# Kernel optimization log

Measured on AMD Instinct MI355X. Metric: run time of the kernel, lower is better.

Reference implementation:

```python
import jax, jax.numpy as jnp
import numpy as np

NC = 5        # num_class
NS = 2        # n_sigma
MAX_ID = 3    # candidate instance ids per class: 1..MAX_ID
W_INST, W_VAR, W_SEED = 1.0, 10.0, 1.0
GRID = 1024   # size of the registered xym buffer
H = W = 768
CLASS_WEIGHT = np.ones((NC,), np.float32)


def _xym(h, w):
    # buffer built at GRID resolution, then sliced [0:h, 0:w] (matches torch)
    base = jnp.linspace(0.0, 1.0, GRID)
    xm = jnp.broadcast_to(base[None, :w], (h, w))  # x varies along width
    ym = jnp.broadcast_to(base[:h, None], (h, w))  # y varies along height
    return jnp.stack([xm, ym], 0)  # [2,h,w]


def _lovasz_flat(logits, labels_f):
    # standard flat Lovasz hinge
    signs = 2.0 * labels_f - 1.0
    errors = 1.0 - logits * signs
    perm = jnp.argsort(-errors)  # descending errors
    errors_sorted = errors[perm]
    gt_sorted = labels_f[perm]
    gts = jnp.sum(gt_sorted)
    inter = gts - jnp.cumsum(gt_sorted)
    union = gts + jnp.cumsum(1.0 - gt_sorted)
    jac = 1.0 - inter / union
    jac = jnp.concatenate([jac[:1], jac[1:] - jac[:-1]])
    return jnp.dot(jax.nn.relu(errors_sorted), jax.lax.stop_gradient(jac))


def _per_image(pred, inst, lab, xyf, cw):
    h, w = lab.shape
    n = h * w
    embf = jnp.tanh(pred[0:2]).reshape(2, n) + xyf          # spatial embedding [2,N]
    sigf = pred[2:2 + NS].reshape(NS, n)                     # sigma [NS,N]
    seedf = jax.nn.sigmoid(pred[2 + NS:2 + NS + NC]).reshape(NC, n)  # seed maps [NC,N]
    labf = lab.reshape(n)
    instf = inst.reshape(n)

    cls = jnp.arange(1, NC + 1)
    # background seed loss per class: sum(seed^2) over pixels where label != cl
    bg = labf[None, :] != cls[:, None]
    seed_bg = jnp.sum(jnp.where(bg, seedf, 0.0) ** 2)

    cl_pair = jnp.repeat(cls, MAX_ID)                       # [P]
    id_pair = jnp.tile(jnp.arange(1, MAX_ID + 1), NC)       # [P]

    def per_inst(cl, iid):
        ci = cl - 1
        m = (labf == cl) & (instf == iid)                   # [N]
        mf = m.astype(embf.dtype)
        cnt = jnp.sum(mf)
        valid = cnt > 0
        cnts = jnp.maximum(cnt, 1.0)
        # approximate medoid: per-dim lower median of masked coords,
        # then masked pixel closest to the median
        xy_sorted = jnp.sort(jnp.where(m[None, :], xyf, 2.0), axis=1)
        mid = jnp.maximum((cnt.astype(jnp.int32) - 1) // 2, 0)
        med = jnp.take(xy_sorted, mid, axis=1)              # [2]
        d = jnp.sum((xyf - med[:, None]) ** 2, axis=0)
        imin = jnp.argmin(jnp.where(m, d, jnp.inf))
        center = jnp.take(xyf, imin, axis=1)                # [2], constant wrt params
        s_mean = jnp.sum(sigf * mf[None, :], axis=1) / cnts  # [NS]
        var = jnp.sum(mf[None, :] * (sigf - jax.lax.stop_gradient(s_mean)[:, None]) ** 2) / (cnts * NS)
        s = jnp.exp(s_mean * 10.0)                           # [NS]
        dist = jnp.exp(-jnp.sum((embf - center[:, None]) ** 2 * s[:, None], axis=0))  # [N]
        lov = _lovasz_flat(dist * 2.0 - 1.0, mf)
        seedc = jnp.take(seedf, ci, axis=0)
        seed_in = jnp.sum(mf * (seedc - jax.lax.stop_gradient(dist)) ** 2)
        return valid, var, lov, seed_in

    valid, var, lov, seed_in = jax.vmap(per_inst)(cl_pair, id_pair)
    vf = valid.astype(embf.dtype)
    objs = jnp.maximum(jnp.sum(vf), 1.0)
    w_pair = jnp.take(cw, cl_pair - 1)
    seed_loss = (seed_bg + jnp.sum(w_pair * seed_in * vf)) / n
    return (W_INST * jnp.sum(lov * vf) / objs
            + W_VAR * jnp.sum(var * vf) / objs
            + W_SEED * seed_loss)


def setup_inputs() -> dict:
    key = jax.random.key(0)
    k1, k2, k3 = jax.random.split(key, 3)
    prediction = jax.random.normal(k1, (2, 2 + NS + NC, H, W), dtype=jnp.float32)
    instances = jax.random.randint(k2, (2, H, W), 0, MAX_ID + 1, dtype=jnp.int32)
    labels = jax.random.randint(k3, (2, H, W), 0, NC + 1, dtype=jnp.int32)
    return {"prediction": prediction, "instances": instances, "labels": labels}


def reference(prediction, instances, labels):
    xyf = _xym(H, W).reshape(2, H * W)
    cw = jnp.asarray(CLASS_WEIGHT)
    losses = jax.vmap(lambda p, i, l: _per_image(p, i, l, xyf, cw))(prediction, instances, labels)
    return jnp.mean(losses)
```

## Files before the change

kernel.cpp:

```cpp
#include <hip/hip_runtime.h>
#include <cstddef>
#include <cstdint>


#define HH 768
#define WW 768
#define NPIX (HH*WW)
#define NCL 5
#define MAXID 3
#define PAIRS (NCL*MAXID)
#define NIMG 2
#define NCH 9
#define BINS 256
#define NSH 8
#define HPXB 1152
#define HNB (NPIX/HPXB)
#define XW 256
#define YH 16
#define TX 3
#define TY 48
#define BPI (TX*TY)
#define ANB 64
#define APXB (NPIX/ANB)

struct WS {
  alignas(8) unsigned int hall8[NSH][NIMG][PAIRS][2][BINS];
  float seedpart[NIMG][PAIRS][64];
  unsigned int lovdone;
  unsigned int zpad0;
  unsigned long long argkey[NIMG][PAIRS];
  float varsum[NIMG][PAIRS];
  float seedin[NIMG][PAIRS];
  float medx[NIMG][PAIRS], medy[NIMG][PAIRS];
  float s0a[NIMG][PAIRS], s1a[NIMG][PAIRS];
  float sm0a[NIMG][PAIRS], sm1a[NIMG][PAIRS];
  float validf[NIMG][PAIRS], cntf[NIMG][PAIRS];
  float lov[NIMG][PAIRS];
  float seedT[NIMG], seedOwn[NIMG];
  unsigned int cnt[NIMG][PAIRS];
  alignas(16) float4 emb4[NIMG][NPIX];
  unsigned char pridx[NIMG][NPIX];
  alignas(64) unsigned short colpart[NIMG][PAIRS][WW][TY];
  alignas(64) unsigned short rowpart[NIMG][PAIRS][HH][TX];
  float sig0part[NIMG][PAIRS][BPI];
  float sig1part[NIMG][PAIRS][BPI];
  float sq0part[NIMG][PAIRS][BPI];
  float sq1part[NIMG][PAIRS][BPI];
  float sTpart[NIMG][BPI];
  float sOpart[NIMG][BPI];
};

__device__ __forceinline__ float basef(int i) {
  return (float)i * (1.0f / 1023.0f);
}
__device__ __forceinline__ int pair_of(int l, int it) {
  return (l >= 1 && l <= NCL && it >= 1 && it <= MAXID) ? (l - 1) * MAXID + (it - 1) : -1;
}
__device__ __forceinline__ float fast_sigmoid(float z) {
  return __fdividef(1.f, 1.f + __expf(-z));
}
__device__ __forceinline__ float fast_tanh(float x) {
  float xc = fminf(fmaxf(x, -15.f), 15.f);
  float e = __expf(2.f * xc);
  return __fdividef(e - 1.f, e + 1.f);
}
__device__ __forceinline__ float vget(float4 v, int k) {
  return (k == 0) ? v.x : (k == 1) ? v.y : (k == 2) ? v.z : v.w;
}
__device__ __forceinline__ int iget(int4 v, int k) {
  return (k == 0) ? v.x : (k == 1) ? v.y : (k == 2) ? v.z : v.w;
}

__global__ __launch_bounds__(512) void k_pass1(const float* __restrict__ pred,
                                               const int* __restrict__ inst,
                                               const int* __restrict__ lab,
                                               WS* __restrict__ ws) {
  int img = blockIdx.z;
  int xt = blockIdx.x, yt = blockIdx.y;
  int x0 = xt * XW;
  int y0 = yt * YH;
  int tid = threadIdx.x, lane = tid & 63, wv = tid >> 6;

  {
    const int ZN = (int)(offsetof(WS, argkey) / 4);
    int bid = (blockIdx.z * TY + blockIdx.y) * TX + blockIdx.x;
    int idx = bid * 512 + tid;
    if (idx < ZN) ((unsigned int*)ws)[idx] = 0u;
    if (bid == 0 && tid < NIMG * PAIRS)
      ((unsigned long long*)ws->argkey)[tid] = ~0ULL;
  }

  const float* p = pred + (size_t)img * NCH * NPIX;
  const int* lb = lab + (size_t)img * NPIX;
  const int* ib = inst + (size_t)img * NPIX;

  __shared__ unsigned int lcol[PAIRS][XW];
  __shared__ unsigned int lrow[PAIRS][YH];
  __shared__ float lsig0[PAIRS], lsig1[PAIRS], lsq0[PAIRS], lsq1[PAIRS];
  __shared__ float fred0[8], fred1[8];
  for (int k = tid; k < PAIRS * XW; k += 512) ((unsigned int*)lcol)[k] = 0;
  for (int k = tid; k < PAIRS * YH; k += 512) ((unsigned int*)lrow)[k] = 0;
  if (tid < PAIRS) { lsig0[tid] = 0.f; lsig1[tid] = 0.f; lsq0[tid] = 0.f; lsq1[tid] = 0.f; }
  __syncthreads();

  int xq = lane;
  float t = 0.f, own = 0.f;
#pragma unroll
  for (int i = 0; i < 2; i++) {
    int r = wv + 8 * i;
    int y = y0 + r;
    int pixb = y * WW + x0 + xq * 4;
    float4 c0 = *(const float4*)(p + 0 * NPIX + pixb);
    float4 c1 = *(const float4*)(p + 1 * NPIX + pixb);
    float4 c2 = *(const float4*)(p + 2 * NPIX + pixb);
    float4 c3 = *(const float4*)(p + 3 * NPIX + pixb);
    float4 c4 = *(const float4*)(p + 4 * NPIX + pixb);
    float4 c5 = *(const float4*)(p + 5 * NPIX + pixb);
    float4 c6 = *(const float4*)(p + 6 * NPIX + pixb);
    float4 c7 = *(const float4*)(p + 7 * NPIX + pixb);
    float4 c8 = *(const float4*)(p + 8 * NPIX + pixb);
    int4 l4 = *(const int4*)(lb + pixb);
    int4 i4 = *(const int4*)(ib + pixb);
    float by = basef(y);
    uchar4 pv;
#pragma unroll
    for (int k = 0; k < 4; k++) {
      int l = iget(l4, k), it = iget(i4, k);
      float s, q, sdown = 0.f;
      s = fast_sigmoid(vget(c4, k)); q = s * s; t += q; if (l == 1) { own += q; sdown = s; }
      s = fast_sigmoid(vget(c5, k)); q = s * s; t += q; if (l == 2) { own += q; sdown = s; }
      s = fast_sigmoid(vget(c6, k)); q = s * s; t += q; if (l == 3) { own += q; sdown = s; }
      s = fast_sigmoid(vget(c7, k)); q = s * s; t += q; if (l == 4) { own += q; sdown = s; }
      s = fast_sigmoid(vget(c8, k)); q = s * s; t += q; if (l == 5) { own += q; sdown = s; }
      float e0 = fast_tanh(vget(c0, k)) + basef(x0 + xq * 4 + k);
      float e1 = fast_tanh(vget(c1, k)) + by;
      int pr = pair_of(l, it);
      float4 rec;
      rec.x = e0; rec.y = e1; rec.z = sdown;
      rec.w = __int_as_float(pr >= 0 ? pr : 255);
      ws->emb4[img][pixb + k] = rec;
      ((unsigned char*)&pv)[k] = (unsigned char)(pr >= 0 ? pr : 255);
      if (pr >= 0) {
        float g0 = vget(c2, k), g1 = vget(c3, k);
        atomicAdd(&lcol[pr][xq * 4 + k], 1u);
        atomicAdd(&lrow[pr][r], 1u);
        atomicAdd(&lsig0[pr], g0);
        atomicAdd(&lsig1[pr], g1);
        atomicAdd(&lsq0[pr], g0 * g0);
        atomicAdd(&lsq1[pr], g1 * g1);
      }
    }
    *(uchar4*)(ws->pridx[img] + pixb) = pv;
  }
  for (int o = 32; o; o >>= 1) { t += __shfl_down(t, o); own += __shfl_down(own, o); }
  if (lane == 0) { fred0[wv] = t; fred1[wv] = own; }
  __syncthreads();

  int bi = yt * TX + xt;
  for (int k = tid; k < PAIRS * XW; k += 512) {
    int pp = k >> 8, c = k & 255;
    ws->colpart[img][pp][x0 + c][yt] = (unsigned short)lcol[pp][c];
  }
  for (int k = tid; k < PAIRS * YH; k += 512) {
    int pp = k / YH, r = k % YH;
    ws->rowpart[img][pp][y0 + r][xt] = (unsigned short)lrow[pp][r];
  }
  if (tid < PAIRS) {
    ws->sig0part[img][tid][bi] = lsig0[tid];
    ws->sig1part[img][tid][bi] = lsig1[tid];
    ws->sq0part[img][tid][bi] = lsq0[tid];
    ws->sq1part[img][tid][bi] = lsq1[tid];
  }
  if (tid == 0) {
    float a = 0.f, b2 = 0.f;
#pragma unroll
    for (int w = 0; w < 8; w++) { a += fred0[w]; b2 += fred1[w]; }
    ws->sTpart[img][bi] = a;
    ws->sOpart[img][bi] = b2;
  }
}

__global__ __launch_bounds__(256) void k_medoid(WS* __restrict__ ws) {
  int img = blockIdx.x / PAIRS, p = blockIdx.x % PAIRS;
  int tid = threadIdx.x, lane = tid & 63, wv = tid >> 6;
  __shared__ unsigned int pref[256];
  __shared__ int cross;
  __shared__ float fr0[4], fr1[4], fr2[4], fr3[4];
  unsigned int c = 0;
  int res[2];
#pragma unroll
  for (int h = 0; h < 2; h++) {
    unsigned int v[3];
#pragma unroll
    for (int j = 0; j < 3; j++) {
      int cc = tid * 3 + j;
      unsigned int s = 0;
      if (h == 0) {
        const unsigned int* w = (const unsigned int*)ws->colpart[img][p][cc];
#pragma unroll
        for (int i = 0; i < TY / 2; i++) { unsigned int u = w[i]; s += (u & 0xFFFFu) + (u >> 16); }
      } else {
        const unsigned short* w = ws->rowpart[img][p][cc];
        s = (unsigned int)w[0] + w[1] + w[2];
      }
      v[j] = s;
    }
    unsigned int s3 = v[0] + v[1] + v[2];
    pref[tid] = s3;
    __syncthreads();
    for (int d = 1; d < 256; d <<= 1) {
      unsigned int tv = (tid >= d) ? pref[tid - d] : 0u;
      __syncthreads();
      pref[tid] += tv;
      __syncthreads();
    }
    c = pref[255];
    unsigned int target = (c > 0) ? (((c - 1u) >> 1) + 1u) : 1u;
    if (tid == 0) cross = 0;
    __syncthreads();
    unsigned int inc = pref[tid];
    unsigned int exc = inc - s3;
    if (inc >= target && exc < target) {
      int j = (exc + v[0] >= target) ? 0 : ((exc + v[0] + v[1] >= target) ? 1 : 2);
      cross = tid * 3 + j;
    }
    __syncthreads();
    res[h] = cross;
    __syncthreads();
  }
  float s0 = 0.f, s1 = 0.f, q0 = 0.f, q1 = 0.f;
  for (int b = tid; b < BPI; b += 256) {
    s0 += ws->sig0part[img][p][b]; s1 += ws->sig1part[img][p][b];
    q0 += ws->sq0part[img][p][b];  q1 += ws->sq1part[img][p][b];
  }
  for (int o = 32; o; o >>= 1) {
    s0 += __shfl_down(s0, o); s1 += __shfl_down(s1, o);
    q0 += __shfl_down(q0, o); q1 += __shfl_down(q1, o);
  }
  if (lane == 0) { fr0[wv] = s0; fr1[wv] = s1; fr2[wv] = q0; fr3[wv] = q1; }
  __syncthreads();
  if (tid == 0) {
    float sig0 = fr0[0] + fr0[1] + fr0[2] + fr0[3];
    float sig1 = fr1[0] + fr1[1] + fr1[2] + fr1[3];
    float sq0 = fr2[0] + fr2[1] + fr2[2] + fr2[3];
    float sq1 = fr3[0] + fr3[1] + fr3[2] + fr3[3];
    float vf = (c > 0) ? 1.f : 0.f;
    float cf = (c > 0) ? (float)c : 1.f;
    float sm0 = sig0 / cf, sm1 = sig1 / cf;
    ws->cnt[img][p] = c;
    ws->medx[img][p] = basef(res[0]);
    ws->medy[img][p] = basef(res[1]);
    ws->sm0a[img][p] = sm0;
    ws->sm1a[img][p] = sm1;
    ws->s0a[img][p] = __expf(10.f * sm0);
    ws->s1a[img][p] = __expf(10.f * sm1);
    ws->validf[img][p] = vf;
    ws->cntf[img][p] = cf;
    ws->varsum[img][p] = (sq0 - cf * sm0 * sm0) + (sq1 - cf * sm1 * sm1);
  }
  __syncthreads();
  if (p == 0) {
    float a = 0.f, o2 = 0.f;
    for (int b = tid; b < BPI; b += 256) { a += ws->sTpart[img][b]; o2 += ws->sOpart[img][b]; }
    for (int o = 32; o; o >>= 1) { a += __shfl_down(a, o); o2 += __shfl_down(o2, o); }
    if (lane == 0) { fr0[wv] = a; fr1[wv] = o2; }
    __syncthreads();
    if (tid == 0) {
      ws->seedT[img] = fr0[0] + fr0[1] + fr0[2] + fr0[3];
      ws->seedOwn[img] = fr1[0] + fr1[1] + fr1[2] + fr1[3];
    }
  }
}

__global__ __launch_bounds__(256) void k_argmin(WS* __restrict__ ws) {
  int img = blockIdx.y;
  __shared__ unsigned long long skey[PAIRS];
  __shared__ float smx[PAIRS], smy[PAIRS];
  if (threadIdx.x < PAIRS) {
    skey[threadIdx.x] = ~0ULL;
    smx[threadIdx.x] = ws->medx[img][threadIdx.x];
    smy[threadIdx.x] = ws->medy[img][threadIdx.x];
  }
  __syncthreads();
  int base = blockIdx.x * APXB;
#pragma unroll
  for (int i = 0; i < APXB / 1024; i++) {
    int px0 = base + i * 1024 + threadIdx.x * 4;
    uchar4 pr4 = *(const uchar4*)(ws->pridx[img] + px0);
    int y = px0 / WW;
    int x0 = px0 - y * WW;
    float by = basef(y);
#pragma unroll
    for (int k = 0; k < 4; k++) {
      int pr = (k == 0) ? pr4.x : (k == 1) ? pr4.y : (k == 2) ? pr4.z : pr4.w;
      if (pr != 255) {
        int pix = px0 + k;
        float dx = basef(x0 + k) - smx[pr];
        float dy = by - smy[pr];
        float d = dx * dx + dy * dy;
        unsigned long long key = ((unsigned long long)__float_as_uint(d) << 32) | (unsigned int)pix;
        atomicMin(&skey[pr], key);
      }
    }
  }
  __syncthreads();
  if (threadIdx.x < PAIRS && skey[threadIdx.x] != ~0ULL)
    atomicMin(&ws->argkey[img][threadIdx.x], skey[threadIdx.x]);
}

__global__ __launch_bounds__(512) void k_hist(WS* __restrict__ ws) {
  int img = blockIdx.y;
  int tid = threadIdx.x;
  __shared__ unsigned int h32[PAIRS * 2 * BINS];
  __shared__ float lseed[PAIRS];
  for (int k = tid; k < PAIRS * 2 * BINS; k += 512) h32[k] = 0;
  if (tid < PAIRS) lseed[tid] = 0.f;
  __syncthreads();

  float cxr[PAIRS], cyr[PAIRS], S0r[PAIRS], S1r[PAIRS];
#pragma unroll
  for (int p = 0; p < PAIRS; p++) {
    unsigned long long key = ws->argkey[img][p];
    int imin = (int)(key & 0xffffffffu);
    cxr[p] = basef(imin % WW);
    cyr[p] = basef(imin / WW);
    S0r[p] = ws->s0a[img][p];
    S1r[p] = ws->s1a[img][p];
  }
  const float4* eb = ws->emb4[img];
  int base = blockIdx.x * HPXB;

  auto hist_px = [&](float4 v) {
    int pp = __float_as_int(v.w);
    float dOwn = 0.f;
#pragma unroll
    for (int p = 0; p < PAIRS; p++) {
      float dx = v.x - cxr[p];
      float dy = v.y - cyr[p];
      float q = dx * dx * S0r[p] + dy * dy * S1r[p];
      float d = __expf(-q);
      bool m = (pp == p);
      dOwn = m ? d : dOwn;
      int ib2 = (int)fminf(d * 256.f, 255.f);
      atomicAdd(&h32[p * 512 + (ib2 ^ (m ? 511 : 0))], 1u);
    }
    if (pp != 255) { float sd = v.z - dOwn; atomicAdd(&lseed[pp], sd * sd); }
  };

  float4 vA = eb[base + tid];
  float4 vB = eb[base + 512 + tid];
  float4 vC;
  bool hasC = tid < (HPXB - 1024);
  if (hasC) vC = eb[base + 1024 + tid];
  hist_px(vA);
  hist_px(vB);
  if (hasC) hist_px(vC);
  __syncthreads();

  unsigned long long* gh = (unsigned long long*)&ws->hall8[blockIdx.x & (NSH - 1)][img][0][0][0];
  for (int k = tid; k < PAIRS * 2 * BINS / 2; k += 512) {
    unsigned int lo = h32[2 * k], hi = h32[2 * k + 1];
    if (lo | hi) {
      unsigned long long v = (unsigned long long)lo | ((unsigned long long)hi << 32);
      atomicAdd(&gh[k], v);
    }
  }
  if (tid < PAIRS && lseed[tid] != 0.f)
    atomicAdd(&ws->seedpart[img][tid][blockIdx.x & 63], lseed[tid]);
}

__global__ __launch_bounds__(256) void k_lovasz(WS* __restrict__ ws, float* __restrict__ out) {
  int b = blockIdx.x / PAIRS, p = blockIdx.x % PAIRS;
  unsigned int gts = ws->cnt[b][p];
  int tid = threadIdx.x;
  float lv = 0.f;
  __shared__ unsigned int sin_s[BINS], sout_s[BINS];
  if (gts != 0) {
    unsigned int si = 0, so = 0;
#pragma unroll
    for (int s = 0; s < NSH; s++) {
      si += ws->hall8[s][b][p][1][tid];
      so += ws->hall8[s][b][p][0][tid];
    }
    sin_s[tid] = si; sout_s[tid] = so;
    __syncthreads();
    for (int d = 1; d < BINS; d <<= 1) {
      unsigned int a = (tid + d < BINS) ? sin_s[tid + d] : 0u;
      unsigned int c = (tid + d < BINS) ? sout_s[tid + d] : 0u;
      __syncthreads();
      sin_s[tid] += a; sout_s[tid] += c;
      __syncthreads();
    }
    float gtsf = (float)gts;
    float js = 0.f;
    if (tid >= 1) {
      unsigned int Sin = sin_s[tid], Sout = sout_s[tid];
      js = 1.f - (float)(gts - Sin) / (gtsf + (float)Sout);
    }
    for (int o = 32; o; o >>= 1) js += __shfl_down(js, o);
    __shared__ float wsum[4];
    if ((tid & 63) == 0) wsum[tid >> 6] = js;
    __syncthreads();
    if (tid == 0)
      lv = (2.f / BINS) * (0.5f + wsum[0] + wsum[1] + wsum[2] + wsum[3]);
  }
  __shared__ float seedred;
  if (tid < 64) {
    float sv = ws->seedpart[b][p][tid];
    for (int o = 32; o; o >>= 1) sv += __shfl_down(sv, o);
    if (tid == 0) seedred = sv;
  }
  __syncthreads();
  __shared__ int amLast;
  if (tid == 0) {
    atomicExch(&ws->lov[b][p], lv);
    atomicExch(&ws->seedin[b][p], seedred);
    __threadfence();
    unsigned int old = atomicAdd(&ws->lovdone, 1u);
    amLast = (old == NIMG * PAIRS - 1);
  }
  __syncthreads();
  if (amLast) {
    __shared__ float rl[NIMG], rv[NIMG], rs[NIMG], ro[NIMG];
    if (tid < NIMG) { rl[tid] = 0.f; rv[tid] = 0.f; rs[tid] = 0.f; ro[tid] = 0.f; }
    __syncthreads();
    if (tid < NIMG * PAIRS) {
      int bb = tid / PAIRS, pp = tid % PAIRS;
      float vf = ws->validf[bb][pp];
      float lvv = atomicAdd(&ws->lov[bb][pp], 0.f);
      float sdv = atomicAdd(&ws->seedin[bb][pp], 0.f);
      atomicAdd(&rl[bb], vf * lvv);
      atomicAdd(&rv[bb], vf * ws->varsum[bb][pp] / (ws->cntf[bb][pp] * 2.f));
      atomicAdd(&rs[bb], vf * sdv);
      atomicAdd(&ro[bb], vf);
    }
    __syncthreads();
    if (tid == 0) {
      float tot = 0.f;
      for (int bb = 0; bb < NIMG; bb++) {
        float objs = ro[bb] < 1.f ? 1.f : ro[bb];
        float seed_bg = ws->seedT[bb] - ws->seedOwn[bb];
        float seed_loss = (seed_bg + rs[bb]) / (float)NPIX;
        tot += rl[bb] / objs + 10.f * rv[bb] / objs + seed_loss;
      }
      out[0] = tot * 0.5f;
    }
  }
}

extern "C" void kernel_launch(void* const* d_in, const int* in_sizes, int n_in,
                              void* d_out, int out_size, void* d_ws, size_t ws_size,
                              hipStream_t stream) {
  const float* pred = (const float*)d_in[0];
  const int* inst = (const int*)d_in[1];
  const int* lab = (const int*)d_in[2];
  WS* ws = (WS*)d_ws;

  k_pass1<<<dim3(TX, TY, NIMG), 512, 0, stream>>>(pred, inst, lab, ws);
  k_medoid<<<dim3(NIMG * PAIRS), 256, 0, stream>>>(ws);
  k_argmin<<<dim3(ANB, NIMG), 256, 0, stream>>>(ws);
  k_hist<<<dim3(HNB, NIMG), 512, 0, stream>>>(ws);
  k_lovasz<<<dim3(NIMG * PAIRS), 256, 0, stream>>>(ws, (float*)d_out);
}
```

Before: 94.06 us.

## Shrink tile height and store column/row partials tile-major with packed writes

Halves the tile height from 16 to 8 rows, doubling the number of tiles so each thread handles one row of four pixels instead of two. The per-tile column and row count partials are now stored tile-major ([tile][pair][x]) and written as packed 32-bit words, replacing the strided scatter into a [pair][x][tile] layout. The medoid kernel now gathers column sums across 96 tile rows with strided 16-bit reads instead of contiguous reads. The aim is to improve occupancy and the coalescing of the first kernel's writes, at the cost of a larger partial buffer and a less coalesced reduction in the medoid kernel.

```diff
diff --git a/kernel.cpp b/kernel.cpp
--- a/kernel.cpp
+++ b/kernel.cpp
@@ -16,9 +16,9 @@
 #define HPXB 1152
 #define HNB (NPIX/HPXB)
 #define XW 256
-#define YH 16
+#define YH 8
 #define TX 3
-#define TY 48
+#define TY 96
 #define BPI (TX*TY)
 #define ANB 64
 #define APXB (NPIX/ANB)
@@ -40,8 +40,8 @@
   unsigned int cnt[NIMG][PAIRS];
   alignas(16) float4 emb4[NIMG][NPIX];
   unsigned char pridx[NIMG][NPIX];
-  alignas(64) unsigned short colpart[NIMG][PAIRS][WW][TY];
-  alignas(64) unsigned short rowpart[NIMG][PAIRS][HH][TX];
+  alignas(4) unsigned short cpart[NIMG][TY][TX][PAIRS][XW];
+  alignas(4) unsigned short rpart[NIMG][TY][TX][PAIRS][YH];
   float sig0part[NIMG][PAIRS][BPI];
   float sig1part[NIMG][PAIRS][BPI];
   float sq0part[NIMG][PAIRS][BPI];
@@ -99,71 +99,73 @@
   __shared__ float lsig0[PAIRS], lsig1[PAIRS], lsq0[PAIRS], lsq1[PAIRS];
   __shared__ float fred0[8], fred1[8];
   for (int k = tid; k < PAIRS * XW; k += 512) ((unsigned int*)lcol)[k] = 0;
-  for (int k = tid; k < PAIRS * YH; k += 512) ((unsigned int*)lrow)[k] = 0;
+  if (tid < PAIRS * YH) ((unsigned int*)lrow)[tid] = 0;
   if (tid < PAIRS) { lsig0[tid] = 0.f; lsig1[tid] = 0.f; lsq0[tid] = 0.f; lsq1[tid] = 0.f; }
   __syncthreads();
 
-  int xq = lane;
+  int r = wv;
+  int y = y0 + r;
+  int xb = lane * 4;
+  int pixb = y * WW + x0 + xb;
+  float4 c0 = *(const float4*)(p + 0 * NPIX + pixb);
+  float4 c1 = *(const float4*)(p + 1 * NPIX + pixb);
+  float4 c2 = *(const float4*)(p + 2 * NPIX + pixb);
+  float4 c3 = *(const float4*)(p + 3 * NPIX + pixb);
+  float4 c4 = *(const float4*)(p + 4 * NPIX + pixb);
+  float4 c5 = *(const float4*)(p + 5 * NPIX + pixb);
+  float4 c6 = *(const float4*)(p + 6 * NPIX + pixb);
+  float4 c7 = *(const float4*)(p + 7 * NPIX + pixb);
+  float4 c8 = *(const float4*)(p + 8 * NPIX + pixb);
+  int4 l4 = *(const int4*)(lb + pixb);
+  int4 i4 = *(const int4*)(ib + pixb);
+  float by = basef(y);
   float t = 0.f, own = 0.f;
-#pragma unroll
-  for (int i = 0; i < 2; i++) {
-    int r = wv + 8 * i;
-    int y = y0 + r;
-    int pixb = y * WW + x0 + xq * 4;
-    float4 c0 = *(const float4*)(p + 0 * NPIX + pixb);
-    float4 c1 = *(const float4*)(p + 1 * NPIX + pixb);
-    float4 c2 = *(const float4*)(p + 2 * NPIX + pixb);
-    float4 c3 = *(const float4*)(p + 3 * NPIX + pixb);
-    float4 c4 = *(const float4*)(p + 4 * NPIX + pixb);
-    float4 c5 = *(const float4*)(p + 5 * NPIX + pixb);
-    float4 c6 = *(const float4*)(p + 6 * NPIX + pixb);
-    float4 c7 = *(const float4*)(p + 7 * NPIX + pixb);
-    float4 c8 = *(const float4*)(p + 8 * NPIX + pixb);
-    int4 l4 = *(const int4*)(lb + pixb);
-    int4 i4 = *(const int4*)(ib + pixb);
-    float by = basef(y);
-    uchar4 pv;
-#pragma unroll
-    for (int k = 0; k < 4; k++) {
-      int l = iget(l4, k), it = iget(i4, k);
-      float s, q, sdown = 0.f;
-      s = fast_sigmoid(vget(c4, k)); q = s * s; t += q; if (l == 1) { own += q; sdown = s; }
-      s = fast_sigmoid(vget(c5, k)); q = s * s; t += q; if (l == 2) { own += q; sdown = s; }
-      s = fast_sigmoid(vget(c6, k)); q = s * s; t += q; if (l == 3) { own += q; sdown = s; }
-      s = fast_sigmoid(vget(c7, k)); q = s * s; t += q; if (l == 4) { own += q; sdown = s; }
-      s = fast_sigmoid(vget(c8, k)); q = s * s; t += q; if (l == 5) { own += q; sdown = s; }
-      float e0 = fast_tanh(vget(c0, k)) + basef(x0 + xq * 4 + k);
-      float e1 = fast_tanh(vget(c1, k)) + by;
-      int pr = pair_of(l, it);
-      float4 rec;
-      rec.x = e0; rec.y = e1; rec.z = sdown;
-      rec.w = __int_as_float(pr >= 0 ? pr : 255);
-      ws->emb4[img][pixb + k] = rec;
-      ((unsigned char*)&pv)[k] = (unsigned char)(pr >= 0 ? pr : 255);
-      if (pr >= 0) {
-        float g0 = vget(c2, k), g1 = vget(c3, k);
-        atomicAdd(&lcol[pr][xq * 4 + k], 1u);
-        atomicAdd(&lrow[pr][r], 1u);
-        atomicAdd(&lsig0[pr], g0);
-        atomicAdd(&lsig1[pr], g1);
-        atomicAdd(&lsq0[pr], g0 * g0);
-        atomicAdd(&lsq1[pr], g1 * g1);
-      }
-    }
-    *(uchar4*)(ws->pridx[img] + pixb) = pv;
-  }
+  uchar4 pv;
+#pragma unroll
+  for (int k = 0; k < 4; k++) {
+    int l = iget(l4, k), it = iget(i4, k);
+    float s, q, sdown = 0.f;
+    s = fast_sigmoid(vget(c4, k)); q = s * s; t += q; if (l == 1) { own += q; sdown = s; }
+    s = fast_sigmoid(vget(c5, k)); q = s * s; t += q; if (l == 2) { own += q; sdown = s; }
+    s = fast_sigmoid(vget(c6, k)); q = s * s; t += q; if (l == 3) { own += q; sdown = s; }
+    s = fast_sigmoid(vget(c7, k)); q = s * s; t += q; if (l == 4) { own += q; sdown = s; }
+    s = fast_sigmoid(vget(c8, k)); q = s * s; t += q; if (l == 5) { own += q; sdown = s; }
+    float e0 = fast_tanh(vget(c0, k)) + basef(x0 + xb + k);
+    float e1 = fast_tanh(vget(c1, k)) + by;
+    int pr = pair_of(l, it);
+    float4 rec;
+    rec.x = e0; rec.y = e1; rec.z = sdown;
+    rec.w = __int_as_float(pr >= 0 ? pr : 255);
+    ws->emb4[img][pixb + k] = rec;
+    ((unsigned char*)&pv)[k] = (unsigned char)(pr >= 0 ? pr : 255);
+    if (pr >= 0) {
+      float g0 = vget(c2, k), g1 = vget(c3, k);
+      atomicAdd(&lcol[pr][xb + k], 1u);
+      atomicAdd(&lrow[pr][r], 1u);
+      atomicAdd(&lsig0[pr], g0);
+      atomicAdd(&lsig1[pr], g1);
+      atomicAdd(&lsq0[pr], g0 * g0);
+      atomicAdd(&lsq1[pr], g1 * g1);
+    }
+  }
+  *(uchar4*)(ws->pridx[img] + pixb) = pv;
+
   for (int o = 32; o; o >>= 1) { t += __shfl_down(t, o); own += __shfl_down(own, o); }
   if (lane == 0) { fred0[wv] = t; fred1[wv] = own; }
   __syncthreads();
 
   int bi = yt * TX + xt;
-  for (int k = tid; k < PAIRS * XW; k += 512) {
-    int pp = k >> 8, c = k & 255;
-    ws->colpart[img][pp][x0 + c][yt] = (unsigned short)lcol[pp][c];
-  }
-  for (int k = tid; k < PAIRS * YH; k += 512) {
-    int pp = k / YH, r = k % YH;
-    ws->rowpart[img][pp][y0 + r][xt] = (unsigned short)lrow[pp][r];
+  unsigned int* cp = (unsigned int*)&ws->cpart[img][yt][xt][0][0];
+  const unsigned int* lc = (const unsigned int*)lcol;
+#pragma unroll
+  for (int k = tid; k < PAIRS * XW / 2; k += 512) {
+    unsigned int lo = lc[2 * k], hi = lc[2 * k + 1];
+    cp[k] = (lo & 0xFFFFu) | (hi << 16);
+  }
+  if (tid < PAIRS * YH / 2) {
+    const unsigned int* lr = (const unsigned int*)lrow;
+    unsigned int lo = lr[2 * tid], hi = lr[2 * tid + 1];
+    ((unsigned int*)&ws->rpart[img][yt][xt][0][0])[tid] = (lo & 0xFFFFu) | (hi << 16);
   }
   if (tid < PAIRS) {
     ws->sig0part[img][tid][bi] = lsig0[tid];
@@ -196,12 +198,14 @@
       int cc = tid * 3 + j;
       unsigned int s = 0;
       if (h == 0) {
-        const unsigned int* w = (const unsigned int*)ws->colpart[img][p][cc];
-#pragma unroll
-        for (int i = 0; i < TY / 2; i++) { unsigned int u = w[i]; s += (u & 0xFFFFu) + (u >> 16); }
+        int xt2 = cc >> 8, ci = cc & 255;
+        for (int yt2 = 0; yt2 < TY; yt2++)
+          s += ws->cpart[img][yt2][xt2][p][ci];
       } else {
-        const unsigned short* w = ws->rowpart[img][p][cc];
-        s = (unsigned int)w[0] + w[1] + w[2];
+        int yt2 = cc >> 3, ri = cc & 7;
+        s = (unsigned int)ws->rpart[img][yt2][0][p][ri]
+          + ws->rpart[img][yt2][1][p][ri]
+          + ws->rpart[img][yt2][2][p][ri];
       }
       v[j] = s;
     }
```

After: 94.60 us. No clear change (+0.6%).
